# Kernel optimization log

Hardware: AMD Instinct MI355X
Metric: run time of the kernel (lower is better)

The kernel has to match this reference:

```python
import jax, jax.numpy as jnp
import numpy as np
from jax import lax

K = 8  # window / output_stride (hardcoded in original forward)
BN_EPS = 1e-5


def setup_inputs() -> dict:
    key = jax.random.key(0)
    ks = jax.random.split(key, 4)
    B, C, H, W = 4, 56, 320, 320
    return {
        "x": jax.random.normal(ks[0], (B, C, H, W), jnp.float32),
        "conv1_w": jax.random.normal(ks[1], (56, 56), jnp.float32) * 0.01,
        "conv1_b": jnp.zeros((56,), jnp.float32),
        "conv2_w": jax.random.normal(ks[2], (1, 56), jnp.float32) * 0.01,
        "conv2_b": jnp.zeros((1,), jnp.float32),
        "bn1_gamma": jnp.ones((56,), jnp.float32),
        "bn1_beta": jnp.zeros((56,), jnp.float32),
        "bn2_gamma": jnp.ones((1,), jnp.float32),
        "bn2_beta": jnp.zeros((1,), jnp.float32),
    }


def _batchnorm(y, gamma, beta):
    # training-mode BatchNorm2d: stats over (N, H, W) per channel
    mean = jnp.mean(y, axis=(0, 2, 3), keepdims=True)
    var = jnp.var(y, axis=(0, 2, 3), keepdims=True)
    yhat = (y - mean) * lax.rsqrt(var + BN_EPS)
    return yhat * gamma[None, :, None, None] + beta[None, :, None, None]


def _counter(x, w1, b1, w2, b2, g1, be1, g2, be2):
    # AvgPool2d(kernel=8, stride=1) -> [B,56,H-7,W-7]
    p = lax.reduce_window(x, 0.0, lax.add, (1, 1, K, K), (1, 1, 1, 1), "VALID") / (K * K)
    y = jnp.einsum("oc,bchw->bohw", w1, p) + b1[None, :, None, None]
    y = jax.nn.relu(_batchnorm(y, g1, be1))
    y = jnp.einsum("oc,bchw->bohw", w2, y) + b2[None, :, None, None]
    y = jax.nn.relu(_batchnorm(y, g2, be2))
    return y  # [B,1,Hc,Wc]


def _dynamic_unfolding(x, local_count):
    # x: [B,C,H,W], local_count: [B,1,H-7,W-7]
    B, C, H, W = x.shape
    Hc, Wc = H - K + 1, W - K + 1
    m = jnp.mean(x, axis=1)  # [B,H,W]
    # extract all 8x8 sliding windows -> [B,Hc,Wc,64]
    patches = jnp.stack(
        [m[:, di:di + Hc, dj:dj + Wc] for di in range(K) for dj in range(K)],
        axis=-1,
    )
    sm = jax.nn.softmax(patches, axis=-1)  # per-window softmax
    wgt = sm * local_count[:, 0, :, :, None]  # [B,Hc,Wc,64]
    # overlapping fold (scatter-add) back to [B,1,H,W]
    R = jnp.zeros((B, H, W), x.dtype)
    for di in range(K):
        for dj in range(K):
            R = R.at[:, di:di + Hc, dj:dj + Wc].add(wgt[..., di * K + dj])
    return R[:, None, :, :]


def reference(x, conv1_w, conv1_b, conv2_w, conv2_b, bn1_gamma, bn1_beta, bn2_gamma, bn2_beta):
    C_out = _counter(x, conv1_w, conv1_b, conv2_w, conv2_b, bn1_gamma, bn1_beta, bn2_gamma, bn2_beta)
    R = _dynamic_unfolding(x, C_out)
    return C_out, R
```

## Files before the change

### kernel.cpp

```cpp
#include <hip/hip_runtime.h>
#include <math.h>

#define B 4
#define C 56
#define H 320
#define W 320
#define HC 313
#define WC 313
#define NIMG (H*W)
#define NSP  (HC*WC)
#define NPIX (B*NSP)
#define NM   (B*NIMG)
#define BN_EPS 1e-5f
#define NGRID 512

#define PHR 39
#define NF4 390

typedef __attribute__((ext_vector_type(8))) short short8;
typedef __attribute__((ext_vector_type(16))) float float16;
typedef __attribute__((ext_vector_type(4))) float f32x4;

__device__ __forceinline__ unsigned short f2bf(float v) {
  unsigned int u = __float_as_uint(v);
  return (unsigned short)((u + 0x7fffu + ((u >> 16) & 1u)) >> 16);
}

__global__ __launch_bounds__(256) void pool32_kernel(
    const float* __restrict__ x, float* __restrict__ Epart,
    unsigned short* __restrict__ p_t) {
  __shared__ float tin[PHR][40];
  __shared__ float hs[PHR][32];
  __shared__ unsigned short Pt[8][1024];
  const int tid = threadIdx.x;
  int bid = blockIdx.x;
  const int g = bid % 7; bid /= 7;
  const int b = bid & 3; bid >>= 2;
  const int ty = bid / 10, tx = bid - (bid / 10) * 10;
  const int i0 = ty * 32, j0 = tx * 32;
  const float* xg = x + ((size_t)b * C + g * 8) * NIMG;

  int r4[2], q4[2]; bool act[2], vld[2], inter[2]; size_t xoff[2];
  #pragma unroll
  for (int k = 0; k < 2; ++k) {
    int idx = tid + k * 256;
    r4[k] = idx / 10; q4[k] = idx - r4[k] * 10;
    act[k] = idx < NF4;
    vld[k] = act[k] && (i0 + r4[k] < H) && (j0 + q4[k] * 4 < W);
    inter[k] = act[k] && r4[k] < 32 && q4[k] < 8;
    xoff[k] = (size_t)(i0 + r4[k]) * W + j0 + q4[k] * 4;
  }
  f32x4 cur4[2], nxt4[2];
  #pragma unroll
  for (int k = 0; k < 2; ++k)
    cur4[k] = vld[k] ? *(const f32x4*)(xg + xoff[k]) : (f32x4){0.f, 0.f, 0.f, 0.f};

  f32x4 esum4[2] = {{0.f, 0.f, 0.f, 0.f}, {0.f, 0.f, 0.f, 0.f}};

  #pragma unroll
  for (int c = 0; c < 8; ++c) {
    #pragma unroll
    for (int k = 0; k < 2; ++k) {
      if (act[k]) *(f32x4*)&tin[r4[k]][q4[k] * 4] = cur4[k];
      if (inter[k]) esum4[k] += cur4[k];
    }
    __syncthreads();
    if (c < 7) {
      const float* xp = xg + (size_t)(c + 1) * NIMG;
      #pragma unroll
      for (int k = 0; k < 2; ++k)
        nxt4[k] = vld[k] ? *(const f32x4*)(xp + xoff[k]) : (f32x4){0.f, 0.f, 0.f, 0.f};
    }
    #pragma unroll
    for (int it = 0; it < 5; ++it) {
      int idx = tid + it * 256;
      if (idx < PHR * 32) {
        int r = idx >> 5, j = idx & 31;
        float s = 0.f;
        #pragma unroll
        for (int d = 0; d < 8; ++d) s += tin[r][j + d];
        hs[r][j] = s;
      }
    }
    __syncthreads();
    #pragma unroll
    for (int it = 0; it < 4; ++it) {
      int idx = tid + it * 256;
      int i = idx >> 5, j = idx & 31;
      float s = 0.f;
      #pragma unroll
      for (int d = 0; d < 8; ++d) s += hs[i + d][j];
      Pt[c][idx] = f2bf(s * (1.f / 64.f));
    }
    #pragma unroll
    for (int k = 0; k < 2; ++k) cur4[k] = nxt4[k];
  }
  __syncthreads();

  float* Eb = Epart + ((size_t)g * B + b) * NIMG;
  #pragma unroll
  for (int k = 0; k < 2; ++k)
    if (inter[k]) *(f32x4*)&Eb[(i0 + r4[k]) * W + j0 + q4[k] * 4] = esum4[k];

  unsigned short* pg = p_t + (size_t)g * NPIX * 8;
  #pragma unroll
  for (int k = 0; k < 4; ++k) {
    int idx = tid + k * 256;
    int i = idx >> 5, j = idx & 31;
    int gi = i0 + i, gj = j0 + j;
    if (gi < HC && gj < WC) {
      unsigned short t8[8];
      #pragma unroll
      for (int c2 = 0; c2 < 8; ++c2) t8[c2] = Pt[c2][idx];
      *(short8*)(pg + ((size_t)b * NSP + gi * WC + gj) * 8) = *(short8*)t8;
    }
  }
}

__global__ __launch_bounds__(256) void se_pool_kernel(
    const float* __restrict__ Epart, float* __restrict__ E, float* __restrict__ S) {
  __shared__ float tin[39][40];
  __shared__ float hs[39][33];
  const int b = blockIdx.z;
  const int i0 = blockIdx.y * 32, j0 = blockIdx.x * 32;
  const int tid = threadIdx.x;
  for (int idx = tid; idx < 39 * 39; idx += 256) {
    int r = idx / 39, cc = idx - r * 39;
    int gi = i0 + r, gj = j0 + cc;
    float v = 0.f;
    if (gi < H && gj < W) {
      float s = 0.f;
      #pragma unroll
      for (int g = 0; g < 7; ++g)
        s += Epart[((size_t)g * B + b) * NIMG + gi * W + gj];
      v = expf(s * (1.f / C));
      if (r < 32 && cc < 32) E[(size_t)b * NIMG + gi * W + gj] = v;
    }
    tin[r][cc] = v;
  }
  __syncthreads();
  for (int idx = tid; idx < 39 * 32; idx += 256) {
    int r = idx >> 5, j = idx & 31;
    float s = 0.f;
    #pragma unroll
    for (int d = 0; d < 8; ++d) s += tin[r][j + d];
    hs[r][j] = s;
  }
  __syncthreads();
  for (int idx = tid; idx < 32 * 32; idx += 256) {
    int i = idx >> 5, j = idx & 31;
    int gi = i0 + i, gj = j0 + j;
    if (gi < HC && gj < WC) {
      float s = 0.f;
      #pragma unroll
      for (int d = 0; d < 8; ++d) s += hs[i + d][j];
      S[(size_t)b * NSP + gi * WC + gj] = s;
    }
  }
}

__global__ __launch_bounds__(256) void y1_stats_kernel(
    const unsigned short* __restrict__ p_t, const float* __restrict__ w1,
    float* __restrict__ ypart) {
  __shared__ unsigned short Wl[64 * 64];
  __shared__ float red[4][32][64];
  const int tid = threadIdx.x, wave = tid >> 6, lane = tid & 63;
  for (int idx = tid; idx < 4096; idx += 256) {
    int o = idx >> 6, k = idx & 63;
    float v = (o < C && k < C) ? w1[o * C + k] : 0.f;
    *(unsigned short*)((char*)Wl + (o * 128 + ((2 * k) ^ ((o & 7) << 4)))) = f2bf(v);
  }
  __syncthreads();
  short8 afr[2][4];
  #pragma unroll
  for (int q = 0; q < 2; ++q)
    #pragma unroll
    for (int ks = 0; ks < 4; ++ks) {
      int row = q * 32 + (lane & 31), kb = ks * 16 + 8 * (lane >> 5);
      afr[q][ks] = *(const short8*)((const char*)Wl + row * 128 + ((2 * kb) ^ ((row & 7) << 4)));
    }
  float s1[2][16], s2[2][16];
  #pragma unroll
  for (int q = 0; q < 2; ++q)
    #pragma unroll
    for (int r = 0; r < 16; ++r) { s1[q][r] = 0.f; s2[q][r] = 0.f; }

  const int h = lane >> 5;
  const int nchunk = (NPIX + 127) / 128;
  for (int ch = blockIdx.x; ch < nchunk; ch += NGRID) {
    int col = ch * 128 + wave * 32 + (lane & 31);
    bool cv = col < NPIX;
    size_t pofs = (size_t)(cv ? col : 0) * 8;
    short8 bfr[4];
    #pragma unroll
    for (int ks = 0; ks < 4; ++ks) {
      int g = ks * 2 + h;
      short8 bv = (short8){0, 0, 0, 0, 0, 0, 0, 0};
      if (g < 7 && cv) bv = *(const short8*)(p_t + (size_t)g * NPIX * 8 + pofs);
      bfr[ks] = bv;
    }
    float16 a0 = {}, a1 = {};
    #pragma unroll
    for (int ks = 0; ks < 4; ++ks) {
      a0 = __builtin_amdgcn_mfma_f32_32x32x16_bf16(afr[0][ks], bfr[ks], a0, 0, 0, 0);
      a1 = __builtin_amdgcn_mfma_f32_32x32x16_bf16(afr[1][ks], bfr[ks], a1, 0, 0, 0);
    }
    #pragma unroll
    for (int r = 0; r < 16; ++r) {
      s1[0][r] += a0[r]; s2[0][r] = fmaf(a0[r], a0[r], s2[0][r]);
      s1[1][r] += a1[r]; s2[1][r] = fmaf(a1[r], a1[r], s2[1][r]);
    }
  }
  for (int pass = 0; pass < 2; ++pass) {
    __syncthreads();
    #pragma unroll
    for (int q = 0; q < 2; ++q)
      #pragma unroll
      for (int r = 0; r < 16; ++r)
        red[wave][q * 16 + r][lane] = pass ? s2[q][r] : s1[q][r];
    __syncthreads();
    if (tid < C) {
      int row = tid, q = row >> 5, rr = row & 31;
      int hh = (rr >> 2) & 1, reg = (rr & 3) | ((rr >> 3) << 2);
      float s = 0.f;
      #pragma unroll
      for (int w = 0; w < 4; ++w)
        #pragma unroll
        for (int cl = 0; cl < 32; ++cl)
          s += red[w][q * 16 + reg][32 * hh + cl];
      ypart[blockIdx.x * 112 + pass * 56 + row] = s;
    }
  }
}

__global__ void ypart_bn1_kernel(const float* __restrict__ ypart,
                                 const float* __restrict__ g1, const float* __restrict__ be1,
                                 float* __restrict__ ac) {
  __shared__ float sums[112];
  int t = threadIdx.x;
  if (t < 112) {
    float s0 = 0.f, s1 = 0.f, s2 = 0.f, s3 = 0.f;
    #pragma unroll 4
    for (int b = 0; b < NGRID; b += 4) {
      s0 += ypart[(b + 0) * 112 + t];
      s1 += ypart[(b + 1) * 112 + t];
      s2 += ypart[(b + 2) * 112 + t];
      s3 += ypart[(b + 3) * 112 + t];
    }
    sums[t] = (s0 + s1) + (s2 + s3);
  }
  __syncthreads();
  if (t < C) {
    float m = sums[t] * (1.f / NPIX);
    float var = sums[56 + t] * (1.f / NPIX) - m * m;
    float a = g1[t] * rsqrtf(var + BN_EPS);
    ac[t] = a;
    ac[C + t] = fmaf(-a, m, be1[t]);
  }
}

__global__ __launch_bounds__(256) void y2_kernel(
    const unsigned short* __restrict__ p_t, const float* __restrict__ w1,
    const float* __restrict__ ac, const float* __restrict__ w2,
    float* __restrict__ y2, float* __restrict__ stats2) {
  __shared__ unsigned short Wl[64 * 64];
  __shared__ float af[64], cf[64], wf[64];
  const int tid = threadIdx.x, wave = tid >> 6, lane = tid & 63;
  for (int idx = tid; idx < 4096; idx += 256) {
    int o = idx >> 6, k = idx & 63;
    float v = (o < C && k < C) ? w1[o * C + k] : 0.f;
    *(unsigned short*)((char*)Wl + (o * 128 + ((2 * k) ^ ((o & 7) << 4)))) = f2bf(v);
  }
  if (tid < 64) {
    bool ok = tid < C;
    af[tid] = ok ? ac[tid] : 0.f;
    cf[tid] = ok ? ac[C + tid] : 0.f;
    wf[tid] = ok ? w2[tid] : 0.f;
  }
  __syncthreads();
  short8 afr[2][4];
  #pragma unroll
  for (int q = 0; q < 2; ++q)
    #pragma unroll
    for (int ks = 0; ks < 4; ++ks) {
      int row = q * 32 + (lane & 31), kb = ks * 16 + 8 * (lane >> 5);
      afr[q][ks] = *(const short8*)((const char*)Wl + row * 128 + ((2 * kb) ^ ((row & 7) << 4)));
    }
  const int h = lane >> 5;
  float ss1 = 0.f, ss2 = 0.f;
  const int nchunk = (NPIX + 127) / 128;
  for (int ch = blockIdx.x; ch < nchunk; ch += NGRID) {
    int col = ch * 128 + wave * 32 + (lane & 31);
    bool cv = col < NPIX;
    size_t pofs = (size_t)(cv ? col : 0) * 8;
    short8 bfr[4];
    #pragma unroll
    for (int ks = 0; ks < 4; ++ks) {
      int g = ks * 2 + h;
      short8 bv = (short8){0, 0, 0, 0, 0, 0, 0, 0};
      if (g < 7 && cv) bv = *(const short8*)(p_t + (size_t)g * NPIX * 8 + pofs);
      bfr[ks] = bv;
    }
    float16 a0 = {}, a1 = {};
    #pragma unroll
    for (int ks = 0; ks < 4; ++ks) {
      a0 = __builtin_amdgcn_mfma_f32_32x32x16_bf16(afr[0][ks], bfr[ks], a0, 0, 0, 0);
      a1 = __builtin_amdgcn_mfma_f32_32x32x16_bf16(afr[1][ks], bfr[ks], a1, 0, 0, 0);
    }
    float ysum = 0.f;
    #pragma unroll
    for (int r = 0; r < 16; ++r) {
      int o0 = (r & 3) + 8 * (r >> 2) + 4 * h;
      ysum = fmaf(wf[o0], fmaxf(fmaf(af[o0], a0[r], cf[o0]), 0.f), ysum);
      int o1 = o0 + 32;
      ysum = fmaf(wf[o1], fmaxf(fmaf(af[o1], a1[r], cf[o1]), 0.f), ysum);
    }
    ysum += __shfl_xor(ysum, 32);
    bool wr = cv && lane < 32;
    if (wr) {
      y2[col] = ysum;
      ss1 += ysum;
      ss2 = fmaf(ysum, ysum, ss2);
    }
  }
  #pragma unroll
  for (int off = 1; off < 64; off <<= 1) {
    ss1 += __shfl_xor(ss1, off);
    ss2 += __shfl_xor(ss2, off);
  }
  if (lane == 0) {
    atomicAdd(&stats2[(blockIdx.x & 63) * 2 + 0], ss1);
    atomicAdd(&stats2[(blockIdx.x & 63) * 2 + 1], ss2);
  }
}

__global__ void bn2_final_kernel(const float* __restrict__ stats2,
                                 const float* __restrict__ g2, const float* __restrict__ be2,
                                 float* __restrict__ a2c2) {
  int t = threadIdx.x;
  float s1 = stats2[t * 2], s2 = stats2[t * 2 + 1];
  #pragma unroll
  for (int off = 32; off > 0; off >>= 1) {
    s1 += __shfl_down(s1, off);
    s2 += __shfl_down(s2, off);
  }
  if (t == 0) {
    float mean = s1 * (1.f / NPIX);
    float var  = s2 * (1.f / NPIX) - mean * mean;
    float a = g2[0] * rsqrtf(var + BN_EPS);
    a2c2[0] = a;
    a2c2[1] = fmaf(-a, mean, be2[0]);
  }
}

__global__ __launch_bounds__(256) void r_pool_kernel(
    const float* __restrict__ y2, const float* __restrict__ S,
    const float* __restrict__ a2c2, const float* __restrict__ E,
    float* __restrict__ cout, float* __restrict__ R) {
  __shared__ float tin[39][40];
  __shared__ float hs[39][33];
  const int b = blockIdx.z;
  const int i0 = blockIdx.y * 32, j0 = blockIdx.x * 32;
  const int tid = threadIdx.x;
  const float a2 = a2c2[0], c2 = a2c2[1];
  const float* y2b = y2 + (size_t)b * NSP;
  const float* Sb  = S + (size_t)b * NSP;
  float* cb = cout + (size_t)b * NSP;
  for (int idx = tid; idx < 39 * 39; idx += 256) {
    int r = idx / 39, cc = idx - r * 39;
    int gi = i0 + r - 7, gj = j0 + cc - 7;
    float t = 0.f;
    if (gi >= 0 && gi < HC && gj >= 0 && gj < WC) {
      float v = fmaxf(fmaf(a2, y2b[gi * WC + gj], c2), 0.f);
      t = v / Sb[gi * WC + gj];
      if (r >= 7 && cc >= 7) cb[gi * WC + gj] = v;
    }
    tin[r][cc] = t;
  }
  __syncthreads();
  for (int idx = tid; idx < 39 * 32; idx += 256) {
    int r = idx >> 5, j = idx & 31;
    float s = 0.f;
    #pragma unroll
    for (int d = 0; d < 8; ++d) s += tin[r][j + d];
    hs[r][j] = s;
  }
  __syncthreads();
  for (int idx = tid; idx < 32 * 32; idx += 256) {
    int i = idx >> 5, j = idx & 31;
    size_t gofs = (size_t)b * NIMG + (i0 + i) * W + (j0 + j);
    float s = 0.f;
    #pragma unroll
    for (int d = 0; d < 8; ++d) s += hs[i + d][j];
    R[gofs] = E[gofs] * s;
  }
}

extern "C" void kernel_launch(void* const* d_in, const int* in_sizes, int n_in,
                              void* d_out, int out_size, void* d_ws, size_t ws_size,
                              hipStream_t stream) {
  const float* x   = (const float*)d_in[0];
  const float* w1  = (const float*)d_in[1];
  const float* w2  = (const float*)d_in[3];
  const float* g1  = (const float*)d_in[5];
  const float* be1 = (const float*)d_in[6];
  const float* g2  = (const float*)d_in[7];
  const float* be2 = (const float*)d_in[8];

  float* out_c = (float*)d_out;
  float* out_r = out_c + NPIX;

  unsigned short* p_t = (unsigned short*)d_ws;
  float* fbase = (float*)(p_t + (size_t)7 * NPIX * 8);
  size_t off = 0;
  float* Epart  = fbase + off; off += (size_t)7 * NM;
  float* E      = fbase + off; off += NM;
  float* Sarr   = fbase + off; off += NPIX;
  float* y2     = fbase + off; off += NPIX;
  float* ypart  = fbase + off; off += (size_t)NGRID * 112;
  float* stats2 = fbase + off; off += 128;
  float* ac     = fbase + off; off += 112;
  float* a2c2   = fbase + off; off += 2;

  hipMemsetAsync(stats2, 0, 128 * sizeof(float), stream);

  pool32_kernel<<<100 * B * 7, 256, 0, stream>>>(x, Epart, p_t);

  dim3 sg(10, 10, B);
  se_pool_kernel<<<sg, 256, 0, stream>>>(Epart, E, Sarr);

  y1_stats_kernel<<<NGRID, 256, 0, stream>>>(p_t, w1, ypart);
  ypart_bn1_kernel<<<1, 128, 0, stream>>>(ypart, g1, be1, ac);
  y2_kernel<<<NGRID, 256, 0, stream>>>(p_t, w1, ac, w2, y2, stats2);
  bn2_final_kernel<<<1, 64, 0, stream>>>(stats2, g2, be2, a2c2);

  dim3 rg(10, 10, B);
  r_pool_kernel<<<rg, 256, 0, stream>>>(y2, Sarr, a2c2, E, out_c, out_r);
}
```

Before: 118.2 us.

## Process two channels per pool iteration and replace BN2 atomics with partial sums

```diff
diff --git a/kernel.cpp b/kernel.cpp
--- a/kernel.cpp
+++ b/kernel.cpp
@@ -29,8 +29,8 @@
 __global__ __launch_bounds__(256) void pool32_kernel(
     const float* __restrict__ x, float* __restrict__ Epart,
     unsigned short* __restrict__ p_t) {
-  __shared__ float tin[PHR][40];
-  __shared__ float hs[PHR][32];
+  __shared__ float tin[2][PHR][40];
+  __shared__ float hs[2][PHR][32];
   __shared__ unsigned short Pt[8][1024];
   const int tid = threadIdx.x;
   int bid = blockIdx.x;
@@ -50,50 +50,64 @@
     inter[k] = act[k] && r4[k] < 32 && q4[k] < 8;
     xoff[k] = (size_t)(i0 + r4[k]) * W + j0 + q4[k] * 4;
   }
-  f32x4 cur4[2], nxt4[2];
-  #pragma unroll
-  for (int k = 0; k < 2; ++k)
-    cur4[k] = vld[k] ? *(const f32x4*)(xg + xoff[k]) : (f32x4){0.f, 0.f, 0.f, 0.f};
+  f32x4 cur4[2][2], nxt4[2][2];
+  #pragma unroll
+  for (int c2 = 0; c2 < 2; ++c2)
+    #pragma unroll
+    for (int k = 0; k < 2; ++k)
+      cur4[c2][k] = vld[k] ? *(const f32x4*)(xg + (size_t)c2 * NIMG + xoff[k])
+                           : (f32x4){0.f, 0.f, 0.f, 0.f};
 
   f32x4 esum4[2] = {{0.f, 0.f, 0.f, 0.f}, {0.f, 0.f, 0.f, 0.f}};
 
   #pragma unroll
-  for (int c = 0; c < 8; ++c) {
+  for (int cc = 0; cc < 8; cc += 2) {
     #pragma unroll
     for (int k = 0; k < 2; ++k) {
-      if (act[k]) *(f32x4*)&tin[r4[k]][q4[k] * 4] = cur4[k];
-      if (inter[k]) esum4[k] += cur4[k];
+      if (act[k]) {
+        *(f32x4*)&tin[0][r4[k]][q4[k] * 4] = cur4[0][k];
+        *(f32x4*)&tin[1][r4[k]][q4[k] * 4] = cur4[1][k];
+      }
+      if (inter[k]) esum4[k] += cur4[0][k] + cur4[1][k];
     }
     __syncthreads();
-    if (c < 7) {
-      const float* xp = xg + (size_t)(c + 1) * NIMG;
-      #pragma unroll
-      for (int k = 0; k < 2; ++k)
-        nxt4[k] = vld[k] ? *(const f32x4*)(xp + xoff[k]) : (f32x4){0.f, 0.f, 0.f, 0.f};
-    }
-    #pragma unroll
-    for (int it = 0; it < 5; ++it) {
+    if (cc < 6) {
+      #pragma unroll
+      for (int c2 = 0; c2 < 2; ++c2)
+        #pragma unroll
+        for (int k = 0; k < 2; ++k)
+          nxt4[c2][k] = vld[k]
+              ? *(const f32x4*)(xg + (size_t)(cc + 2 + c2) * NIMG + xoff[k])
+              : (f32x4){0.f, 0.f, 0.f, 0.f};
+    }
+    #pragma unroll
+    for (int it = 0; it < 10; ++it) {
       int idx = tid + it * 256;
-      if (idx < PHR * 32) {
-        int r = idx >> 5, j = idx & 31;
+      if (idx < 2 * PHR * 32) {
+        int ch = idx >= PHR * 32;
+        int rem = idx - ch * PHR * 32;
+        int r = rem >> 5, j = rem & 31;
         float s = 0.f;
         #pragma unroll
-        for (int d = 0; d < 8; ++d) s += tin[r][j + d];
-        hs[r][j] = s;
+        for (int d = 0; d < 8; ++d) s += tin[ch][r][j + d];
+        hs[ch][r][j] = s;
       }
     }
     __syncthreads();
     #pragma unroll
-    for (int it = 0; it < 4; ++it) {
+    for (int it = 0; it < 8; ++it) {
       int idx = tid + it * 256;
-      int i = idx >> 5, j = idx & 31;
+      int ch = idx >> 10, pl = idx & 1023;
+      int i = pl >> 5, j = pl & 31;
       float s = 0.f;
       #pragma unroll
-      for (int d = 0; d < 8; ++d) s += hs[i + d][j];
-      Pt[c][idx] = f2bf(s * (1.f / 64.f));
-    }
-    #pragma unroll
-    for (int k = 0; k < 2; ++k) cur4[k] = nxt4[k];
+      for (int d = 0; d < 8; ++d) s += hs[ch][i + d][j];
+      Pt[cc + ch][pl] = f2bf(s * (1.f / 64.f));
+    }
+    #pragma unroll
+    for (int c2 = 0; c2 < 2; ++c2)
+      #pragma unroll
+      for (int k = 0; k < 2; ++k) cur4[c2][k] = nxt4[c2][k];
   }
   __syncthreads();
 
@@ -262,7 +276,7 @@
 __global__ __launch_bounds__(256) void y2_kernel(
     const unsigned short* __restrict__ p_t, const float* __restrict__ w1,
     const float* __restrict__ ac, const float* __restrict__ w2,
-    float* __restrict__ y2, float* __restrict__ stats2) {
+    float* __restrict__ y2, float* __restrict__ y2part) {
   __shared__ unsigned short Wl[64 * 64];
   __shared__ float af[64], cf[64], wf[64];
   const int tid = threadIdx.x, wave = tid >> 6, lane = tid & 63;
@@ -329,22 +343,32 @@
     ss2 += __shfl_xor(ss2, off);
   }
   if (lane == 0) {
-    atomicAdd(&stats2[(blockIdx.x & 63) * 2 + 0], ss1);
-    atomicAdd(&stats2[(blockIdx.x & 63) * 2 + 1], ss2);
-  }
-}
-
-__global__ void bn2_final_kernel(const float* __restrict__ stats2,
+    y2part[(blockIdx.x * 4 + wave) * 2 + 0] = ss1;
+    y2part[(blockIdx.x * 4 + wave) * 2 + 1] = ss2;
+  }
+}
+
+__global__ void bn2_final_kernel(const float* __restrict__ y2part,
                                  const float* __restrict__ g2, const float* __restrict__ be2,
                                  float* __restrict__ a2c2) {
+  __shared__ float red[8];
   int t = threadIdx.x;
-  float s1 = stats2[t * 2], s2 = stats2[t * 2 + 1];
+  float s1 = 0.f, s2 = 0.f;
+  for (int i = t; i < NGRID * 4; i += 256) {
+    s1 += y2part[i * 2 + 0];
+    s2 += y2part[i * 2 + 1];
+  }
   #pragma unroll
   for (int off = 32; off > 0; off >>= 1) {
     s1 += __shfl_down(s1, off);
     s2 += __shfl_down(s2, off);
   }
+  int wave = t >> 6, lane = t & 63;
+  if (lane == 0) { red[wave * 2] = s1; red[wave * 2 + 1] = s2; }
+  __syncthreads();
   if (t == 0) {
+    s1 = red[0] + red[2] + red[4] + red[6];
+    s2 = red[1] + red[3] + red[5] + red[7];
     float mean = s1 * (1.f / NPIX);
     float var  = s2 * (1.f / NPIX) - mean * mean;
     float a = g2[0] * rsqrtf(var + BN_EPS);
@@ -418,12 +442,10 @@
   float* Sarr   = fbase + off; off += NPIX;
   float* y2     = fbase + off; off += NPIX;
   float* ypart  = fbase + off; off += (size_t)NGRID * 112;
-  float* stats2 = fbase + off; off += 128;
+  float* y2part = fbase + off; off += (size_t)NGRID * 8;
   float* ac     = fbase + off; off += 112;
   float* a2c2   = fbase + off; off += 2;
 
-  hipMemsetAsync(stats2, 0, 128 * sizeof(float), stream);
-
   pool32_kernel<<<100 * B * 7, 256, 0, stream>>>(x, Epart, p_t);
 
   dim3 sg(10, 10, B);
@@ -431,8 +453,8 @@
 
   y1_stats_kernel<<<NGRID, 256, 0, stream>>>(p_t, w1, ypart);
   ypart_bn1_kernel<<<1, 128, 0, stream>>>(ypart, g1, be1, ac);
-  y2_kernel<<<NGRID, 256, 0, stream>>>(p_t, w1, ac, w2, y2, stats2);
-  bn2_final_kernel<<<1, 64, 0, stream>>>(stats2, g2, be2, a2c2);
+  y2_kernel<<<NGRID, 256, 0, stream>>>(p_t, w1, ac, w2, y2, y2part);
+  bn2_final_kernel<<<1, 256, 0, stream>>>(y2part, g2, be2, a2c2);
 
   dim3 rg(10, 10, B);
   r_pool_kernel<<<rg, 256, 0, stream>>>(y2, Sarr, a2c2, E, out_c, out_r);
```

Measured after the change: 107.3 us. 9.3% less time.
